# Performance work log

Measured on AMD Instinct MI355X. Metric: run time of the kernel, lower is better.

The kernel has to match this reference:

```python
import jax, jax.numpy as jnp
import numpy as np

B, L, E, H = 4, 2048, 512, 8


def setup_inputs() -> dict:
    key = jax.random.key(0)
    ks = jax.random.split(key, 12)
    s = 0.02
    inp = {
        "values": jax.random.normal(ks[0], (B, L, E), jnp.float32),
        "keys": jax.random.normal(ks[1], (B, L, E), jnp.float32),
        "queries": jax.random.normal(ks[2], (B, L, E), jnp.float32),
    }
    mask = jax.random.randint(ks[3], (B, L, H, H), 0, 2, jnp.int32)
    # guarantee at least one unmasked entry per softmax row to avoid NaN rows
    mask = mask.at[..., 0].set(1)
    inp["mask"] = mask
    # Linear(E, E*H) weights stored as (in, out); torch uses y = x @ W.T + b
    inp["Wv"] = jax.random.normal(ks[4], (E, E * H), jnp.float32) * s
    inp["bv"] = jnp.zeros((E * H,), jnp.float32)
    inp["Wk"] = jax.random.normal(ks[5], (E, E * H), jnp.float32) * s
    inp["bk"] = jnp.zeros((E * H,), jnp.float32)
    inp["Wq"] = jax.random.normal(ks[6], (E, E * H), jnp.float32) * s
    inp["bq"] = jnp.zeros((E * H,), jnp.float32)
    inp["Wo"] = jax.random.normal(ks[7], (E * H, E), jnp.float32) * s
    inp["bo"] = jnp.zeros((E,), jnp.float32)
    return inp


def reference(values, keys, queries, mask, Wv, bv, Wk, bk, Wq, bq, Wo, bo):
    b, l, e = queries.shape
    h = Wq.shape[1] // e

    def proj(x, W, bias):
        # (B,L,E) -> (B,L,H,E) -> transpose(1,2) -> (B,H,L,E)
        return (x @ W + bias).reshape(b, -1, h, e).transpose(0, 2, 1, 3)

    v = proj(values, Wv, bv)
    k = proj(keys, Wk, bk)
    q = proj(queries, Wq, bq)
    # Faithful to source: einsum labels applied to the TRANSPOSED (B,H,L,E)
    # tensors, so 'q'/'k' bind to the heads axis and 'h' binds to seq axis.
    # energy: (B, L, H, H) -- head-vs-head scores at each position.
    energy = jnp.einsum('nqhd,nkhd->nhqk', q, k)
    energy = jnp.where(mask == 0, -jnp.inf, energy)
    attn = jax.nn.softmax(energy / jnp.sqrt(jnp.float32(e)), axis=3)
    # out of einsum: (B, H, L, E); raw row-major reshape to (B, L, H*E)
    out = jnp.einsum('nhql,nlhd->nqhd', attn, v).reshape(b, -1, h * e)
    return out @ Wo + bo
```

## Files before the change

kernel.cpp:

```cpp
#include <hip/hip_runtime.h>
#include <stdint.h>

typedef __attribute__((ext_vector_type(4))) float f32x4;
typedef __attribute__((ext_vector_type(8))) __bf16 bf16x8;

__device__ __forceinline__ unsigned short f2bf(float f) {
  union { float f; uint32_t u; } v; v.f = f;
  uint32_t u = v.u;
  return (unsigned short)((u + 0x7FFFu + ((u >> 16) & 1u)) >> 16);
}
__device__ __forceinline__ float bflo(uint32_t u) {
  union { uint32_t u; float f; } v; v.u = u << 16; return v.f;
}
__device__ __forceinline__ float bfhi(uint32_t u) {
  union { uint32_t u; float f; } v; v.u = u & 0xffff0000u; return v.f;
}

__device__ __forceinline__ void async_copy16(void* lds, const void* g) {
  __builtin_amdgcn_global_load_lds(
      (const __attribute__((address_space(1))) void*)g,
      (__attribute__((address_space(3))) void*)lds,
      16, 0, 0);
}

__global__ void cvt3_f32_bf16(const float* __restrict__ in0,
                              const float* __restrict__ in1,
                              const float* __restrict__ in2,
                              uint32_t* __restrict__ out, int n) {
  const float* in = (blockIdx.y == 0) ? in0 : (blockIdx.y == 1) ? in1 : in2;
  uint32_t* o = out + (size_t)blockIdx.y * (n / 2);
  int i = blockIdx.x * blockDim.x + threadIdx.x;
  int idx = i * 8;
  if (idx >= n) return;
  float4 a = *(const float4*)(in + idx);
  float4 b = *(const float4*)(in + idx + 4);
  uint4 ov;
  ov.x = f2bf(a.x) | ((uint32_t)f2bf(a.y) << 16);
  ov.y = f2bf(a.z) | ((uint32_t)f2bf(a.w) << 16);
  ov.z = f2bf(b.x) | ((uint32_t)f2bf(b.y) << 16);
  ov.w = f2bf(b.z) | ((uint32_t)f2bf(b.w) << 16);
  *(uint4*)(o + i * 4) = ov;
}

__global__ void transpose3_to_bf16(const float* __restrict__ in0,
                                   const float* __restrict__ in1,
                                   const float* __restrict__ in2,
                                   unsigned short* __restrict__ out,
                                   int R, int C) {
  const float* in = (blockIdx.z == 0) ? in0 : (blockIdx.z == 1) ? in1 : in2;
  unsigned short* o = out + (size_t)blockIdx.z * ((size_t)R * C);
  __shared__ float tile[32][33];
  int c0 = blockIdx.x * 32, r0 = blockIdx.y * 32;
  int tx = threadIdx.x, ty = threadIdx.y;
  #pragma unroll
  for (int rr = 0; rr < 32; rr += 8)
    tile[ty + rr][tx] = in[(size_t)(r0 + ty + rr) * C + c0 + tx];
  __syncthreads();
  #pragma unroll
  for (int rr = 0; rr < 32; rr += 8)
    o[(size_t)(c0 + ty + rr) * R + r0 + tx] = f2bf(tile[tx][ty + rr]);
}

__global__ void transpose_to_bf16(const float* __restrict__ in,
                                  unsigned short* __restrict__ out,
                                  int R, int C) {
  __shared__ float tile[32][33];
  int c0 = blockIdx.x * 32, r0 = blockIdx.y * 32;
  int tx = threadIdx.x, ty = threadIdx.y;
  #pragma unroll
  for (int rr = 0; rr < 32; rr += 8)
    tile[ty + rr][tx] = in[(size_t)(r0 + ty + rr) * C + c0 + tx];
  __syncthreads();
  #pragma unroll
  for (int rr = 0; rr < 32; rr += 8)
    out[(size_t)(c0 + ty + rr) * R + r0 + tx] = f2bf(tile[tx][ty + rr]);
}

template <int NK, int NN, bool PARTIAL, bool DUAL>
__global__ __launch_bounds__(512, 2) void gemm256(
    const unsigned short* __restrict__ A,
    const unsigned short* __restrict__ Bt,
    const float* __restrict__ bias,
    void* __restrict__ Cout,
    const unsigned short* __restrict__ A2,
    const unsigned short* __restrict__ Bt2,
    const float* __restrict__ bias2,
    void* __restrict__ Cout2,
    int Mt, int NtG, int KC, int Kfull) {
  constexpr int TT = NK * NN;
  static_assert(TT >= 4, "schedule needs >=4 tiles");
  __shared__ unsigned short lds[2 * 2 * 256 * 64];

  const int nwg = Mt * NtG * KC;
  const int cpx = nwg >> 3;
  const int bid = blockIdx.x;
  const int nb = (bid & 7) * cpx + (bid >> 3);
  const int kc = nb / (Mt * NtG);
  const int r2 = nb % (Mt * NtG);
  const int bm = r2 / NtG;
  const int ng = r2 % NtG;
  const int mat = DUAL ? (ng >> 3) : 0;
  const int ngm = DUAL ? (ng & 7) : ng;
  const int N = (DUAL ? (NtG >> 1) : NtG) * NN * 256;
  const size_t koff = (size_t)kc * (NK * 64);

  const unsigned short* Asrc = (DUAL && mat) ? A2 : A;
  const unsigned short* Bsrc = (DUAL && mat) ? Bt2 : Bt;
  const float* biasd = (DUAL && mat) ? bias2 : bias;
  void* Cd = (DUAL && mat) ? Cout2 : Cout;

  const int tid = threadIdx.x;
  const int wv = tid >> 6, ln = tid & 63;
  const int wm = wv >> 2, wn = wv & 3;

  f32x4 acc[8][4] = {};
  bf16x8 af[4][2];
  bf16x8 bfb[2][2];

  auto stage_A = [&](int h, int tau) {
    const int kt = tau % NK;
    #pragma unroll
    for (int r = 0; r < 2; ++r) {
      const int rb = r * 128 + h * 64 + wv * 8;
      const int row = rb + (ln >> 3);
      const int kcs = (ln & 7) ^ (row & 7);
      const unsigned short* g =
          Asrc + (size_t)(bm * 256 + row) * Kfull + koff + kt * 64 + kcs * 8;
      char* dst = (char*)lds + (size_t)(tau & 1) * 65536 + rb * 128;
      async_copy16(dst, g);
    }
  };
  auto stage_B = [&](int h, int tau) {
    const int kt = tau % NK;
    const int bnn = ngm * NN + tau / NK;
    #pragma unroll
    for (int r = 0; r < 2; ++r) {
      const int s = r * 2 + (wv >> 2);
      const int rb = s * 64 + h * 32 + (wv & 3) * 8;
      const int row = rb + (ln >> 3);
      const int kcs = (ln & 7) ^ (row & 7);
      const unsigned short* g =
          Bsrc + (size_t)(bnn * 256 + row) * Kfull + koff + kt * 64 + kcs * 8;
      char* dst = (char*)lds + (size_t)(tau & 1) * 65536 + 32768 + rb * 128;
      async_copy16(dst, g);
    }
  };
  auto load_af = [&](int mh, const char* buf) {
    #pragma unroll
    for (int f = 0; f < 4; ++f) {
      const int lr = wm * 128 + (mh * 4 + f) * 16 + (ln & 15);
      #pragma unroll
      for (int s = 0; s < 2; ++s) {
        const int kq = s * 4 + (ln >> 4);
        af[f][s] = *(const bf16x8*)(buf + lr * 128 + ((kq ^ (lr & 7)) * 16));
      }
    }
  };
  auto load_bf = [&](int nh, const char* buf) {
    #pragma unroll
    for (int gq = 0; gq < 2; ++gq) {
      const int lr = wn * 64 + (nh * 2 + gq) * 16 + (ln & 15);
      #pragma unroll
      for (int s = 0; s < 2; ++s) {
        const int kq = s * 4 + (ln >> 4);
        bfb[gq][s] =
            *(const bf16x8*)(buf + 32768 + lr * 128 + ((kq ^ (lr & 7)) * 16));
      }
    }
  };
  auto mfma_quad = [&](int mh, int nh) {
    __builtin_amdgcn_sched_barrier(0);
    __builtin_amdgcn_s_barrier();
    __builtin_amdgcn_sched_barrier(0);
    __builtin_amdgcn_s_setprio(1);
    #pragma unroll
    for (int f = 0; f < 4; ++f)
      #pragma unroll
      for (int gq = 0; gq < 2; ++gq)
        #pragma unroll
        for (int s = 0; s < 2; ++s)
          acc[mh * 4 + f][nh * 2 + gq] = __builtin_amdgcn_mfma_f32_16x16x32_bf16(
              bfb[gq][s], af[f][s], acc[mh * 4 + f][nh * 2 + gq], 0, 0, 0);
    __builtin_amdgcn_s_setprio(0);
    __builtin_amdgcn_sched_barrier(0);
  };
  auto epilogue = [&](int nt) {
    const int m0 = bm * 256 + wm * 128 + (ln & 15);
    const int n0 = (ngm * NN + nt) * 256 + wn * 64 + ((ln >> 4) << 2);
    if (PARTIAL) {
      float* Cp = (float*)Cd + (size_t)kc * ((size_t)Mt * 256) * N;
      #pragma unroll
      for (int f = 0; f < 8; ++f) {
        const int row = m0 + f * 16;
        #pragma unroll
        for (int g = 0; g < 4; ++g)
          *(f32x4*)(Cp + (size_t)row * N + n0 + g * 16) = acc[f][g];
      }
    } else {
      unsigned short* C = (unsigned short*)Cd;
      #pragma unroll
      for (int f = 0; f < 8; ++f) {
        const int row = m0 + f * 16;
        #pragma unroll
        for (int g = 0; g < 4; ++g) {
          const int col = n0 + g * 16;
          float4 bv = *(const float4*)(biasd + col);
          uint2 o;
          o.x = f2bf(acc[f][g][0] + bv.x) | ((uint32_t)f2bf(acc[f][g][1] + bv.y) << 16);
          o.y = f2bf(acc[f][g][2] + bv.z) | ((uint32_t)f2bf(acc[f][g][3] + bv.w) << 16);
          *(uint2*)(C + (size_t)row * N + col) = o;
        }
      }
    }
    #pragma unroll
    for (int f = 0; f < 8; ++f)
      #pragma unroll
      for (int g = 0; g < 4; ++g)
        acc[f][g] = (f32x4){0.f, 0.f, 0.f, 0.f};
  };

  stage_A(0, 0); stage_B(1, 0); stage_A(1, 0); stage_B(0, 0);
  stage_A(0, 1); stage_B(1, 1); stage_A(1, 1);
  asm volatile("s_waitcnt vmcnt(6)" ::: "memory");
  __builtin_amdgcn_sched_barrier(0);
  __builtin_amdgcn_s_barrier();

  for (int tau = 0; tau < TT; ++tau) {
    const char* buf = (const char*)lds + (size_t)(tau & 1) * 65536;
    load_af(0, buf); load_bf(0, buf);
    if (tau + 1 < TT) stage_B(0, tau + 1);
    mfma_quad(0, 0);
    __builtin_amdgcn_s_barrier();
    load_bf(1, buf);
    if (tau + 2 < TT) stage_A(0, tau + 2);
    mfma_quad(0, 1);
    __builtin_amdgcn_s_barrier();
    load_af(1, buf);
    if (tau + 2 < TT) stage_B(1, tau + 2);
    mfma_quad(1, 1);
    __builtin_amdgcn_s_barrier();
    load_bf(0, buf);
    if (tau + 2 < TT) stage_A(1, tau + 2);
    mfma_quad(1, 0);
    if (tau + 2 < TT) {
      asm volatile("s_waitcnt vmcnt(6)" ::: "memory");
    } else if (tau + 1 < TT) {
      asm volatile("s_waitcnt vmcnt(0)" ::: "memory");
    }
    __builtin_amdgcn_sched_barrier(0);
    __builtin_amdgcn_s_barrier();
    if ((tau + 1) % NK == 0) epilogue(tau / NK);
  }
}

template <int NK>
__global__ __launch_bounds__(256, 2) void gemm128(
    const unsigned short* __restrict__ A,
    const unsigned short* __restrict__ Bt,
    const float* __restrict__ bias,
    unsigned short* __restrict__ Cout,
    int Mt, int Nt, int Kfull) {
  static_assert((NK % 2) == 0, "even NK");
  __shared__ unsigned short lds[2 * 2 * 128 * 64];
  const int nwg = Mt * Nt;
  const int cpx = nwg >> 3;
  const int bid = blockIdx.x;
  const int nb = (bid & 7) * cpx + (bid >> 3);
  const int bm = nb / Nt, bn = nb % Nt;
  const int N = Nt * 128;
  const int tid = threadIdx.x;
  const int wv = tid >> 6, ln = tid & 63;
  const int wm = wv >> 1, wn = wv & 1;

  f32x4 acc[4][4] = {};
  bf16x8 af[4][2], bfb[4][2];
  char* const lds0 = (char*)lds;
  char* const lds1 = (char*)lds + 32768;

  auto stage = [&](int t, char* dst) {
    #pragma unroll
    for (int r = 0; r < 4; ++r) {
      const int c = wv * 4 + r;
      const int row = c * 8 + (ln >> 3);
      const int kcs = (ln & 7) ^ (row & 7);
      const unsigned short* ga =
          A + (size_t)(bm * 128 + row) * Kfull + t * 64 + kcs * 8;
      async_copy16(dst + c * 1024, ga);
      const unsigned short* gb =
          Bt + (size_t)(bn * 128 + row) * Kfull + t * 64 + kcs * 8;
      async_copy16(dst + 16384 + c * 1024, gb);
    }
  };
  auto tile_body = [&](int t, const char* buf, char* obuf) {
    if (t + 1 < NK) stage(t + 1, obuf);
    #pragma unroll
    for (int f = 0; f < 4; ++f) {
      const int lr = wm * 64 + f * 16 + (ln & 15);
      #pragma unroll
      for (int s = 0; s < 2; ++s) {
        const int kq = s * 4 + (ln >> 4);
        af[f][s] = *(const bf16x8*)(buf + lr * 128 + ((kq ^ (lr & 7)) * 16));
      }
    }
    #pragma unroll
    for (int c = 0; c < 4; ++c) {
      const int lr = wn * 64 + c * 16 + (ln & 15);
      #pragma unroll
      for (int s = 0; s < 2; ++s) {
        const int kq = s * 4 + (ln >> 4);
        bfb[c][s] = *(const bf16x8*)(buf + 16384 + lr * 128 + ((kq ^ (lr & 7)) * 16));
      }
    }
    __builtin_amdgcn_s_setprio(1);
    #pragma unroll
    for (int f = 0; f < 4; ++f)
      #pragma unroll
      for (int c = 0; c < 4; ++c)
        #pragma unroll
        for (int s = 0; s < 2; ++s)
          acc[f][c] = __builtin_amdgcn_mfma_f32_16x16x32_bf16(
              bfb[c][s], af[f][s], acc[f][c], 0, 0, 0);
    __builtin_amdgcn_s_setprio(0);
    asm volatile("s_waitcnt vmcnt(0)" ::: "memory");
    __builtin_amdgcn_sched_barrier(0);
    __builtin_amdgcn_s_barrier();
  };

  stage(0, lds0);
  asm volatile("s_waitcnt vmcnt(0)" ::: "memory");
  __builtin_amdgcn_sched_barrier(0);
  __builtin_amdgcn_s_barrier();

  for (int it = 0; it < NK / 2; ++it) {
    tile_body(2 * it,     lds0, lds1);
    tile_body(2 * it + 1, lds1, lds0);
  }

  const int m0 = bm * 128 + wm * 64 + (ln & 15);
  const int n0 = bn * 128 + wn * 64 + ((ln >> 4) << 2);
  #pragma unroll
  for (int f = 0; f < 4; ++f) {
    const int row = m0 + f * 16;
    #pragma unroll
    for (int c = 0; c < 4; ++c) {
      const int col = n0 + c * 16;
      float4 bv = *(const float4*)(bias + col);
      uint2 o;
      o.x = f2bf(acc[f][c][0] + bv.x) | ((uint32_t)f2bf(acc[f][c][1] + bv.y) << 16);
      o.y = f2bf(acc[f][c][2] + bv.z) | ((uint32_t)f2bf(acc[f][c][3] + bv.w) << 16);
      *(uint2*)(Cout + (size_t)row * N + col) = o;
    }
  }
}

__global__ void reduce4_bias(const float* __restrict__ p,
                             const float* __restrict__ bo,
                             float* __restrict__ out) {
  const size_t S = (size_t)8192 * 512;
  size_t i = ((size_t)blockIdx.x * 256 + threadIdx.x) * 4;
  float4 a = *(const float4*)(p + i);
  float4 b = *(const float4*)(p + S + i);
  float4 c = *(const float4*)(p + 2 * S + i);
  float4 d = *(const float4*)(p + 3 * S + i);
  float4 bb = *(const float4*)(bo + (int)(i & 511));
  float4 o;
  o.x = a.x + b.x + c.x + d.x + bb.x;
  o.y = a.y + b.y + c.y + d.y + bb.y;
  o.z = a.z + b.z + c.z + d.z + bb.z;
  o.w = a.w + b.w + c.w + d.w + bb.w;
  *(float4*)(out + i) = o;
}

__global__ __launch_bounds__(256) void energy_mfma(
    const unsigned short* __restrict__ Q,
    const unsigned short* __restrict__ Kb,
    const int* __restrict__ mask,
    float* __restrict__ P) {
  const int wave = threadIdx.x >> 6, ln = threadIdx.x & 63;
  const int t2 = (blockIdx.x * 4 + wave) * 2;
  const int r16 = ln & 15;
  const int g = ln >> 4;
  const size_t rowoff = (size_t)(t2 + (r16 >> 3)) * 4096 + (r16 & 7) * 512 + g * 8;
  const unsigned short* qb = Q + rowoff;
  const unsigned short* kb = Kb + rowoff;

  f32x4 acc = {};
  #pragma unroll
  for (int s = 0; s < 16; ++s) {
    bf16x8 qf = *(const bf16x8*)(qb + s * 32);
    bf16x8 kf = *(const bf16x8*)(kb + s * 32);
    acc = __builtin_amdgcn_mfma_f32_16x16x32_bf16(qf, kf, acc, 0, 0, 0);
  }

  const int ct = r16 >> 3, j = r16 & 7;
  const bool valid = ((g >> 1) == ct);
  const int tok = t2 + ct;
  float pv[4];
  #pragma unroll
  for (int r = 0; r < 4; ++r) {
    const int i = (g & 1) * 4 + r;
    float e = acc[r] * 0.044194173824159216f;
    int mk = 1;
    if (valid) mk = mask[(size_t)tok * 64 + i * 8 + j];
    if (mk == 0) e = -1e30f;
    float m = e;
    m = fmaxf(m, __shfl_xor(m, 1, 64));
    m = fmaxf(m, __shfl_xor(m, 2, 64));
    m = fmaxf(m, __shfl_xor(m, 4, 64));
    float p = __expf(e - m);
    float sum = p;
    sum += __shfl_xor(sum, 1, 64);
    sum += __shfl_xor(sum, 2, 64);
    sum += __shfl_xor(sum, 4, 64);
    pv[r] = p / sum;
  }
  if (valid) {
    #pragma unroll
    for (int r = 0; r < 4; ++r) {
      const int i = (g & 1) * 4 + r;
      P[(size_t)tok * 64 + i * 8 + j] = pv[r];
    }
  }
}

__global__ __launch_bounds__(256) void pv_kernel(
    const float* __restrict__ P,
    const unsigned short* __restrict__ Vb,
    unsigned short* __restrict__ out2) {
  const int wave = threadIdx.x >> 6, lane = threadIdx.x & 63;
  const int t = blockIdx.x * 4 + wave;
  const unsigned short* Vr = Vb + (size_t)t * 4096;
  float att = P[(size_t)t * 64 + lane];

  uint4 v4[8];
  #pragma unroll
  for (int jj = 0; jj < 8; ++jj)
    v4[jj] = *(const uint4*)(Vr + jj * 512 + lane * 8);

  const int nb = t >> 11, l = t & 2047;
  const size_t tok_base = (size_t)nb * 8388608 + (size_t)(l >> 3) * 4096 +
                          (size_t)(l & 7) * 512 + lane * 8;
  #pragma unroll
  for (int hh = 0; hh < 8; ++hh) {
    float accv[8] = {0.f, 0.f, 0.f, 0.f, 0.f, 0.f, 0.f, 0.f};
    #pragma unroll
    for (int jj = 0; jj < 8; ++jj) {
      float a = __shfl(att, hh * 8 + jj, 64);
      accv[0] += a * bflo(v4[jj].x); accv[1] += a * bfhi(v4[jj].x);
      accv[2] += a * bflo(v4[jj].y); accv[3] += a * bfhi(v4[jj].y);
      accv[4] += a * bflo(v4[jj].z); accv[5] += a * bfhi(v4[jj].z);
      accv[6] += a * bflo(v4[jj].w); accv[7] += a * bfhi(v4[jj].w);
    }
    uint4 o;
    o.x = f2bf(accv[0]) | ((uint32_t)f2bf(accv[1]) << 16);
    o.y = f2bf(accv[2]) | ((uint32_t)f2bf(accv[3]) << 16);
    o.z = f2bf(accv[4]) | ((uint32_t)f2bf(accv[5]) << 16);
    o.w = f2bf(accv[6]) | ((uint32_t)f2bf(accv[7]) << 16);
    *(uint4*)(out2 + tok_base + (size_t)hh * 1048576) = o;
  }
}

extern "C" void kernel_launch(void* const* d_in, const int* in_sizes, int n_in,
                              void* d_out, int out_size, void* d_ws, size_t ws_size,
                              hipStream_t stream) {
  const float* values  = (const float*)d_in[0];
  const float* keys    = (const float*)d_in[1];
  const float* queries = (const float*)d_in[2];
  const int*   mask    = (const int*)d_in[3];
  const float* Wv = (const float*)d_in[4];
  const float* bv = (const float*)d_in[5];
  const float* Wk = (const float*)d_in[6];
  const float* bk = (const float*)d_in[7];
  const float* Wq = (const float*)d_in[8];
  const float* bq = (const float*)d_in[9];
  const float* Wo = (const float*)d_in[10];
  const float* bo = (const float*)d_in[11];

  unsigned short* xv  = (unsigned short*)d_ws;
  unsigned short* xk  = xv + 8192 * 512;
  unsigned short* xq  = xk + 8192 * 512;
  unsigned short* Wvt = xq + 8192 * 512;
  unsigned short* Wkt = Wvt + 4096 * 512;
  unsigned short* Wqt = Wkt + 4096 * 512;
  unsigned short* Wot = Wqt + 4096 * 512;
  float*          P   = (float*)(Wot + 4096 * 512);
  unsigned short* bufA = (unsigned short*)(P + 8192 * 64);
  unsigned short* bufB = bufA + (size_t)8192 * 4096;

  const int nx = 8192 * 512;
  cvt3_f32_bf16<<<dim3(nx / 8 / 256, 3), 256, 0, stream>>>(
      values, keys, queries, (uint32_t*)xv, nx);

  transpose3_to_bf16<<<dim3(4096 / 32, 512 / 32, 3), dim3(32, 8), 0, stream>>>(
      Wv, Wk, Wq, Wvt, 512, 4096);
  transpose_to_bf16<<<dim3(512 / 32, 4096 / 32), dim3(32, 8), 0, stream>>>(
      Wo, Wot, 4096, 512);

  gemm256<8, 2, false, true><<<512, 512, 0, stream>>>(
      xq, Wqt, bq, bufA, xk, Wkt, bk, bufB, 32, 16, 1, 512);

  energy_mfma<<<8192 / 8, 256, 0, stream>>>(bufA, bufB, mask, P);

  gemm128<8><<<2048, 256, 0, stream>>>(xv, Wvt, bv, bufA, 64, 32, 512);

  pv_kernel<<<8192 / 4, 256, 0, stream>>>(P, bufA, bufB);

  gemm256<16, 1, true, false><<<256, 512, 0, stream>>>(
      bufB, Wot, nullptr, (float*)bufA, nullptr, nullptr, nullptr, nullptr,
      32, 2, 4, 4096);
  reduce4_bias<<<4096, 256, 0, stream>>>((float*)bufA, bo, (float*)d_out);
}
```

Before: 274.0 us.

## Replace V-projection GEMM with 256x256-tile 16-wave workgroup kernel

The V projection GEMM moves from 128x128 tiles with 4 waves per block to 256x256 tiles with 16 waves per block (1024 threads, 128 KB LDS double buffer). Each staged A/B tile is reused by more waves, which cuts global and L2 traffic per output. A barrier now sits after the LDS fragment reads so the next stage can be overwritten safely, and the trailing wait and barrier are skipped on the last tile. The cost is one block per CU, fewer blocks overall, and more waves contending at each barrier.

After: 362.5 us. +32.3%, slower.

```diff
diff --git a/kernel.cpp b/kernel.cpp
--- a/kernel.cpp
+++ b/kernel.cpp
@@ -254,41 +254,39 @@
 }
 
 template <int NK>
-__global__ __launch_bounds__(256, 2) void gemm128(
+__global__ __launch_bounds__(1024, 1) void gemm16w(
     const unsigned short* __restrict__ A,
     const unsigned short* __restrict__ Bt,
     const float* __restrict__ bias,
     unsigned short* __restrict__ Cout,
     int Mt, int Nt, int Kfull) {
-  static_assert((NK % 2) == 0, "even NK");
-  __shared__ unsigned short lds[2 * 2 * 128 * 64];
+  static_assert((NK % 2) == 0 && NK >= 2, "even NK");
+  __shared__ unsigned short lds[2 * 2 * 256 * 64];
   const int nwg = Mt * Nt;
   const int cpx = nwg >> 3;
   const int bid = blockIdx.x;
   const int nb = (bid & 7) * cpx + (bid >> 3);
   const int bm = nb / Nt, bn = nb % Nt;
-  const int N = Nt * 128;
+  const int N = Nt * 256;
   const int tid = threadIdx.x;
   const int wv = tid >> 6, ln = tid & 63;
-  const int wm = wv >> 1, wn = wv & 1;
+  const int wm = wv >> 2, wn = wv & 3;
 
   f32x4 acc[4][4] = {};
   bf16x8 af[4][2], bfb[4][2];
   char* const lds0 = (char*)lds;
-  char* const lds1 = (char*)lds + 32768;
+  char* const lds1 = (char*)lds + 65536;
 
   auto stage = [&](int t, char* dst) {
     #pragma unroll
-    for (int r = 0; r < 4; ++r) {
-      const int c = wv * 4 + r;
-      const int row = c * 8 + (ln >> 3);
+    for (int r = 0; r < 2; ++r) {
+      const int rb = r * 128 + wv * 8;
+      const int row = rb + (ln >> 3);
       const int kcs = (ln & 7) ^ (row & 7);
-      const unsigned short* ga =
-          A + (size_t)(bm * 128 + row) * Kfull + t * 64 + kcs * 8;
-      async_copy16(dst + c * 1024, ga);
-      const unsigned short* gb =
-          Bt + (size_t)(bn * 128 + row) * Kfull + t * 64 + kcs * 8;
-      async_copy16(dst + 16384 + c * 1024, gb);
+      async_copy16(dst + rb * 128,
+                   A + (size_t)(bm * 256 + row) * Kfull + t * 64 + kcs * 8);
+      async_copy16(dst + 32768 + rb * 128,
+                   Bt + (size_t)(bn * 256 + row) * Kfull + t * 64 + kcs * 8);
     }
   };
   auto tile_body = [&](int t, const char* buf, char* obuf) {
@@ -301,16 +299,16 @@
         const int kq = s * 4 + (ln >> 4);
         af[f][s] = *(const bf16x8*)(buf + lr * 128 + ((kq ^ (lr & 7)) * 16));
       }
-    }
-    #pragma unroll
-    for (int c = 0; c < 4; ++c) {
-      const int lr = wn * 64 + c * 16 + (ln & 15);
+      const int lrb = wn * 64 + f * 16 + (ln & 15);
       #pragma unroll
       for (int s = 0; s < 2; ++s) {
         const int kq = s * 4 + (ln >> 4);
-        bfb[c][s] = *(const bf16x8*)(buf + 16384 + lr * 128 + ((kq ^ (lr & 7)) * 16));
+        bfb[f][s] = *(const bf16x8*)(buf + 32768 + lrb * 128 + ((kq ^ (lrb & 7)) * 16));
       }
     }
+    __builtin_amdgcn_sched_barrier(0);
+    __builtin_amdgcn_s_barrier();
+    __builtin_amdgcn_sched_barrier(0);
     __builtin_amdgcn_s_setprio(1);
     #pragma unroll
     for (int f = 0; f < 4; ++f)
@@ -321,9 +319,12 @@
           acc[f][c] = __builtin_amdgcn_mfma_f32_16x16x32_bf16(
               bfb[c][s], af[f][s], acc[f][c], 0, 0, 0);
     __builtin_amdgcn_s_setprio(0);
-    asm volatile("s_waitcnt vmcnt(0)" ::: "memory");
-    __builtin_amdgcn_sched_barrier(0);
-    __builtin_amdgcn_s_barrier();
+    __builtin_amdgcn_sched_barrier(0);
+    if (t + 1 < NK) {
+      asm volatile("s_waitcnt vmcnt(0)" ::: "memory");
+      __builtin_amdgcn_sched_barrier(0);
+      __builtin_amdgcn_s_barrier();
+    }
   };
 
   stage(0, lds0);
@@ -336,8 +337,8 @@
     tile_body(2 * it + 1, lds1, lds0);
   }
 
-  const int m0 = bm * 128 + wm * 64 + (ln & 15);
-  const int n0 = bn * 128 + wn * 64 + ((ln >> 4) << 2);
+  const int m0 = bm * 256 + wm * 64 + (ln & 15);
+  const int n0 = bn * 256 + wn * 64 + ((ln >> 4) << 2);
   #pragma unroll
   for (int f = 0; f < 4; ++f) {
     const int row = m0 + f * 16;
@@ -501,7 +502,7 @@
 
   energy_mfma<<<8192 / 8, 256, 0, stream>>>(bufA, bufB, mask, P);
 
-  gemm128<8><<<2048, 256, 0, stream>>>(xv, Wvt, bv, bufA, 64, 32, 512);
+  gemm16w<8><<<512, 1024, 0, stream>>>(xv, Wvt, bv, bufA, 32, 16, 512);
 
   pv_kernel<<<8192 / 4, 256, 0, stream>>>(P, bufA, bufB);
 
```
